# Kernel tuning notes

Measured on AMD Instinct MI355X. Metric: run time of the kernel, lower is better.

Reference implementation:

```python
import jax, jax.numpy as jnp
import numpy as np

N_NODES = 50000
N_EDGES = 800000
IN_DIM = 64
HID = 64
NUM_GRAPHS = 512


def _gcn_conv(x, W, b, row, col, norm, n):
    # PyG GCNConv: h = x @ W; out[col] += norm * h[row]; out += b
    h = x @ W  # [N, HID]
    msg = h[row] * norm[:, None]  # [E', HID]
    out = jax.ops.segment_sum(msg, col, num_segments=n)
    return out + b


def setup_inputs() -> dict:
    key = jax.random.key(0)
    ks = jax.random.split(key, 12)
    x = jax.random.normal(ks[0], (N_NODES, IN_DIM), dtype=jnp.float32)
    edge_index = jax.random.randint(ks[1], (2, N_EDGES), 0, N_NODES, dtype=jnp.int64)
    batch = jnp.sort(jax.random.randint(ks[2], (N_NODES,), 0, NUM_GRAPHS, dtype=jnp.int64))
    s = 0.05
    W1 = jax.random.normal(ks[3], (IN_DIM, HID), dtype=jnp.float32) * s
    b1 = jnp.zeros((HID,), dtype=jnp.float32)
    W2 = jax.random.normal(ks[4], (HID, HID), dtype=jnp.float32) * s
    b2 = jnp.zeros((HID,), dtype=jnp.float32)
    W3 = jax.random.normal(ks[5], (HID, HID), dtype=jnp.float32) * s
    b3 = jnp.zeros((HID,), dtype=jnp.float32)
    lin_W = jax.random.normal(ks[6], (HID, 1), dtype=jnp.float32) * s
    lin_b = jnp.zeros((1,), dtype=jnp.float32)
    return {"x": x, "W1": W1, "b1": b1, "W2": W2, "b2": b2, "W3": W3,
            "b3": b3, "lin_W": lin_W, "lin_b": lin_b,
            "edge_index": edge_index, "batch": batch}


def reference(x, W1, b1, W2, b2, W3, b3, lin_W, lin_b, edge_index, batch):
    n = x.shape[0]
    # add self-loops (GCNConv default add_self_loops=True)
    loop = jnp.arange(n, dtype=edge_index.dtype)
    row = jnp.concatenate([edge_index[0], loop])  # source
    col = jnp.concatenate([edge_index[1], loop])  # target (aggregation index)
    # symmetric degree normalization: deg over targets with unit weights
    deg = jax.ops.segment_sum(jnp.ones_like(col, dtype=x.dtype), col, num_segments=n)
    dinv = jnp.where(deg > 0, jax.lax.rsqrt(deg), 0.0)
    norm = dinv[row] * dinv[col]  # [E+N]

    h = jax.nn.relu(_gcn_conv(x, W1, b1, row, col, norm, n))
    h = jax.nn.relu(_gcn_conv(h, W2, b2, row, col, norm, n))
    h = _gcn_conv(h, W3, b3, row, col, norm, n)

    # global_mean_pool over batch ids
    sums = jax.ops.segment_sum(h, batch, num_segments=NUM_GRAPHS)
    cnt = jax.ops.segment_sum(jnp.ones((n,), dtype=h.dtype), batch, num_segments=NUM_GRAPHS)
    pooled = sums / jnp.maximum(cnt, 1.0)[:, None]
    # dropout p=0.5 is identity in eval mode
    return pooled @ lin_W + lin_b  # [NUM_GRAPHS, 1]
```

## Files before the change

kernel.cpp:

```cpp
#include <hip/hip_runtime.h>
#include <hip/hip_fp16.h>

#define NN 50000
#define NE 800000
#define HD 64
#define NG 512
#define NBK 196
#define NBL 196
#define M_CNT (NBK * NBL)
#define NBS 151
#define GEMM_BLOCKS 3125


__global__ void zero_kernel(int* __restrict__ p, int n) {
    int i = blockIdx.x * blockDim.x + threadIdx.x;
    if (i < n) p[i] = 0;
}

__global__ __launch_bounds__(256) void bucket_count(const int* __restrict__ col,
                                                    const int* __restrict__ batch,
                                                    int* __restrict__ counts,
                                                    int* __restrict__ beg,
                                                    int* __restrict__ endx) {
    __shared__ int hist[256];
    int tid = threadIdx.x, blk = blockIdx.x;
    hist[tid] = 0;
    __syncthreads();
    int base = blk * 4096;
#pragma unroll
    for (int k = 0; k < 16; ++k) {
        int e = base + k * 256 + tid;
        if (e < NE) atomicAdd(&hist[col[e] >> 8], 1);
    }
    int t = blk * 256 + tid;
    if (t < NN) {
        int g = batch[t];
        if (t == 0 || batch[t - 1] != g) beg[g] = t;
        if (t == NN - 1 || batch[t + 1] != g) endx[g] = t + 1;
    }
    __syncthreads();
    if (tid < NBK) counts[tid * NBL + blk] = hist[tid];
}

__global__ __launch_bounds__(256) void block_reduce(const int* __restrict__ src,
                                                    int* __restrict__ bsum) {
    __shared__ int ws[4];
    int tid = threadIdx.x, lane = tid & 63, wid = tid >> 6;
    int i = blockIdx.x * 256 + tid;
    int v = (i < M_CNT) ? src[i] : 0;
#pragma unroll
    for (int off = 32; off > 0; off >>= 1) v += __shfl_down(v, off, 64);
    if (lane == 0) ws[wid] = v;
    __syncthreads();
    if (tid == 0) bsum[blockIdx.x] = ws[0] + ws[1] + ws[2] + ws[3];
}

__global__ __launch_bounds__(64) void scan_bsum(int* __restrict__ bsum) {
    int lane = threadIdx.x;
    int carry = 0;
    for (int base = 0; base < NBS; base += 64) {
        int i = base + lane;
        int v = (i < NBS) ? bsum[i] : 0;
        int inc = v;
#pragma unroll
        for (int off = 1; off < 64; off <<= 1) {
            int t = __shfl_up(inc, off, 64);
            if (lane >= off) inc += t;
        }
        if (i < NBS) bsum[i] = carry + inc - v;
        carry += __shfl(inc, 63, 64);
    }
}

__global__ __launch_bounds__(256) void block_scan(const int* __restrict__ src,
                                                  const int* __restrict__ bsum,
                                                  int* __restrict__ dst) {
    __shared__ int ws[4];
    int tid = threadIdx.x, lane = tid & 63, wid = tid >> 6;
    int i = blockIdx.x * 256 + tid;
    int v = (i < M_CNT) ? src[i] : 0;
    int inc = v;
#pragma unroll
    for (int off = 1; off < 64; off <<= 1) {
        int t = __shfl_up(inc, off, 64);
        if (lane >= off) inc += t;
    }
    if (lane == 63) ws[wid] = inc;
    __syncthreads();
    int woff = 0;
    for (int k = 0; k < wid; ++k) woff += ws[k];
    if (i < M_CNT) dst[i] = bsum[blockIdx.x] + woff + inc - v;
}

__global__ __launch_bounds__(256) void gemm1_scatter(const float* __restrict__ x,
                                                     const float* __restrict__ W1,
                                                     __half* __restrict__ h16,
                                                     const int* __restrict__ row,
                                                     const int* __restrict__ col,
                                                     const int* __restrict__ counts_ex,
                                                     unsigned* __restrict__ packed) {
    if (blockIdx.x < GEMM_BLOCKS) {
        __shared__ float Ws[64][64];
        __shared__ float Is[16][64];
        int t = threadIdx.x;
        for (int i = t; i < 64 * 64; i += 256) Ws[i >> 6][i & 63] = W1[i];
        int row0 = blockIdx.x * 16;
        for (int i = t; i < 16 * 64; i += 256)
            Is[i >> 6][i & 63] = x[(row0 + (i >> 6)) * HD + (i & 63)];
        __syncthreads();
        int c = t & 63, r4 = t >> 6;
        float a0 = 0.f, a1 = 0.f, a2 = 0.f, a3 = 0.f;
#pragma unroll
        for (int k = 0; k < 64; ++k) {
            float w = Ws[k][c];
            a0 += Is[r4 + 0][k] * w;
            a1 += Is[r4 + 4][k] * w;
            a2 += Is[r4 + 8][k] * w;
            a3 += Is[r4 + 12][k] * w;
        }
        h16[(row0 + r4 + 0) * HD + c] = __float2half(a0);
        h16[(row0 + r4 + 4) * HD + c] = __float2half(a1);
        h16[(row0 + r4 + 8) * HD + c] = __float2half(a2);
        h16[(row0 + r4 + 12) * HD + c] = __float2half(a3);
    } else {
        __shared__ int cur[256];
        int tid = threadIdx.x, blk = blockIdx.x - GEMM_BLOCKS;
        cur[tid] = 0;
        __syncthreads();
        int base = blk * 4096;
#pragma unroll
        for (int k = 0; k < 16; ++k) {
            int e = base + k * 256 + tid;
            if (e < NE) {
                int c = col[e], r = row[e];
                int b = c >> 8;
                int lpos = atomicAdd(&cur[b], 1);
                int pos = counts_ex[b * NBL + blk] + lpos;
                packed[pos] = (unsigned)r | ((unsigned)(c & 255) << 16);
            }
        }
    }
}

__global__ __launch_bounds__(256) void csr_rowptr(const unsigned* __restrict__ packed,
                                                  const int* __restrict__ counts_ex,
                                                  int* __restrict__ rowptr,
                                                  float* __restrict__ dinv) {
    __shared__ int hist[256];
    __shared__ int ws[4];
    int bkt = blockIdx.x, tid = threadIdx.x;
    int s = counts_ex[bkt * NBL];
    int e = (bkt == NBK - 1) ? NE : counts_ex[(bkt + 1) * NBL];
    hist[tid] = 0;
    __syncthreads();
    for (int j = s + tid; j < e; j += 256)
        atomicAdd(&hist[(packed[j] >> 16) & 255], 1);
    __syncthreads();
    int lane = tid & 63, wid = tid >> 6;
    int v = hist[tid], inc = v;
#pragma unroll
    for (int off = 1; off < 64; off <<= 1) {
        int t = __shfl_up(inc, off, 64);
        if (lane >= off) inc += t;
    }
    if (lane == 63) ws[wid] = inc;
    __syncthreads();
    int woff = 0;
    for (int k = 0; k < wid; ++k) woff += ws[k];
    int node = bkt * 256 + tid;
    if (node < NN) {
        rowptr[node] = s + woff + inc - v;
        dinv[node] = rsqrtf((float)(v + 1));
    }
    if (bkt == 0 && tid == 0) rowptr[NN] = NE;
}

__global__ __launch_bounds__(256) void csr_fill(const unsigned* __restrict__ packed,
                                                const int* __restrict__ counts_ex,
                                                const int* __restrict__ rowptr,
                                                int* __restrict__ esrc) {
    __shared__ int cur[256];
    int bkt = blockIdx.x, tid = threadIdx.x;
    int s = counts_ex[bkt * NBL];
    int e = (bkt == NBK - 1) ? NE : counts_ex[(bkt + 1) * NBL];
    cur[tid] = 0;
    __syncthreads();
    for (int j = s + tid; j < e; j += 256) {
        unsigned p = packed[j];
        int lc = (p >> 16) & 255;
        int slot = rowptr[(bkt << 8) | lc] + atomicAdd(&cur[lc], 1);
        esrc[slot] = (int)(p & 0xFFFF);
    }
}

__global__ __launch_bounds__(256) void gemm64_f16(const __half* __restrict__ in,
                                                  const float* __restrict__ W,
                                                  __half* __restrict__ out) {
    __shared__ float Ws[64][64];
    __shared__ float Is[16][64];
    int t = threadIdx.x;
    for (int i = t; i < 64 * 64; i += 256) Ws[i >> 6][i & 63] = W[i];
    int row0 = blockIdx.x * 16;
    const __half2* in2 = (const __half2*)(in + (size_t)row0 * HD);
    for (int i = t; i < 16 * 32; i += 256) {
        float2 v = __half22float2(in2[i]);
        int r = i >> 5, c2 = (i & 31) * 2;
        Is[r][c2]     = fmaxf(v.x, 0.f);
        Is[r][c2 + 1] = fmaxf(v.y, 0.f);
    }
    __syncthreads();
    int c = t & 63, r4 = t >> 6;
    float a0 = 0.f, a1 = 0.f, a2 = 0.f, a3 = 0.f;
#pragma unroll
    for (int k = 0; k < 64; ++k) {
        float w = Ws[k][c];
        a0 += Is[r4 + 0][k] * w;
        a1 += Is[r4 + 4][k] * w;
        a2 += Is[r4 + 8][k] * w;
        a3 += Is[r4 + 12][k] * w;
    }
    out[(row0 + r4 + 0) * HD + c] = __float2half(a0);
    out[(row0 + r4 + 4) * HD + c] = __float2half(a1);
    out[(row0 + r4 + 8) * HD + c] = __float2half(a2);
    out[(row0 + r4 + 12) * HD + c] = __float2half(a3);
}

template <bool POOL>
__global__ __launch_bounds__(256) void gather_s(const __half* __restrict__ hp,
                                                const int* __restrict__ rowptr,
                                                const int* __restrict__ esrc,
                                                const float* __restrict__ dinv,
                                                const float* __restrict__ b,
                                                __half* __restrict__ out16,
                                                const int* __restrict__ batch,
                                                float* __restrict__ pooled) {
    int tid = threadIdx.x, lane = tid & 63, wid = tid >> 6;
    int hh = lane >> 5, c = lane & 31;
    int node = blockIdx.x * 4 + wid;
    const __half2* hv = (const __half2*)hp;
    int s = rowptr[node], e = rowptr[node + 1];
    int deg = e - s;
    float2 acc = {0.f, 0.f};
    for (int k = 0; k < deg; k += 64) {
        int my = esrc[s + k + lane] & 0xFFFF;
        float myw = dinv[my];
        int nk = min(deg - k, 64);
        int nmain = nk >> 3;
        for (int j = 0; j < nmain; ++j) {
            int t = j * 8 + hh;
            int s0 = __shfl(my, t, 64);
            int s1 = __shfl(my, t + 2, 64);
            int s2 = __shfl(my, t + 4, 64);
            int s3 = __shfl(my, t + 6, 64);
            float w0 = __shfl(myw, t, 64);
            float w1 = __shfl(myw, t + 2, 64);
            float w2 = __shfl(myw, t + 4, 64);
            float w3 = __shfl(myw, t + 6, 64);
            float2 f0 = __half22float2(hv[s0 * 32 + c]);
            float2 f1 = __half22float2(hv[s1 * 32 + c]);
            float2 f2 = __half22float2(hv[s2 * 32 + c]);
            float2 f3 = __half22float2(hv[s3 * 32 + c]);
            acc.x += w0 * f0.x + w1 * f1.x + w2 * f2.x + w3 * f3.x;
            acc.y += w0 * f0.y + w1 * f1.y + w2 * f2.y + w3 * f3.y;
        }
        int tbase = (nk & ~7) + hh;
#pragma unroll
        for (int u = 0; u < 4; ++u) {
            int t = tbase + 2 * u;
            int sl = __shfl(my, t & 63, 64);
            float w = __shfl(myw, t & 63, 64);
            float wm = (t < nk) ? w : 0.f;
            float2 f = __half22float2(hv[sl * 32 + c]);
            acc.x += wm * f.x;
            acc.y += wm * f.y;
        }
    }
    acc.x += __shfl_xor(acc.x, 32, 64);
    acc.y += __shfl_xor(acc.y, 32, 64);
    if (hh == 0) {
        float di = dinv[node];
        float2 self = __half22float2(hv[node * 32 + c]);
        float2 bb = ((const float2*)b)[c];
        float vx = di * acc.x + di * di * self.x + bb.x;
        float vy = di * acc.y + di * di * self.y + bb.y;
        if (POOL) {
            int g = batch[node];
            atomicAdd(&pooled[g * HD + 2 * c], vx);
            atomicAdd(&pooled[g * HD + 2 * c + 1], vy);
        } else {
            ((__half2*)out16)[node * 32 + c] = __floats2half2_rn(vx, vy);
        }
    }
}

__global__ __launch_bounds__(64) void final_kernel(const float* __restrict__ pooled,
                                                   const int* __restrict__ beg,
                                                   const int* __restrict__ endx,
                                                   const float* __restrict__ lin_W,
                                                   const float* __restrict__ lin_b,
                                                   float* __restrict__ out) {
    int g = blockIdx.x, d = threadIdx.x;
    float cnt = (float)(endx[g] - beg[g]);
    float v = pooled[g * HD + d] / fmaxf(cnt, 1.f) * lin_W[d];
#pragma unroll
    for (int off = 32; off > 0; off >>= 1) v += __shfl_down(v, off, 64);
    if (d == 0) out[g] = v + lin_b[0];
}

extern "C" void kernel_launch(void* const* d_in, const int* in_sizes, int n_in,
                              void* d_out, int out_size, void* d_ws, size_t ws_size,
                              hipStream_t stream) {
    const float* x     = (const float*)d_in[0];
    const float* W1    = (const float*)d_in[1];
    const float* b1    = (const float*)d_in[2];
    const float* W2    = (const float*)d_in[3];
    const float* b2    = (const float*)d_in[4];
    const float* W3    = (const float*)d_in[5];
    const float* b3    = (const float*)d_in[6];
    const float* lin_W = (const float*)d_in[7];
    const float* lin_b = (const float*)d_in[8];
    const int* edge_index = (const int*)d_in[9];
    const int* batch      = (const int*)d_in[10];
    const int* row = edge_index;
    const int* col = edge_index + NE;
    float* out = (float*)d_out;

    __half*   h16       = (__half*)d_ws;
    __half*   A16       = h16 + (size_t)NN * HD;
    int*      esrc      = (int*)(A16 + (size_t)NN * HD);
    unsigned* packed    = (unsigned*)(esrc + NE + 64);
    int*      counts    = (int*)(packed + NE);
    int*      counts_ex = counts + M_CNT;
    int*      rowptr    = counts_ex + M_CNT;
    float*    dinv      = (float*)(rowptr + NN + 2);
    int*      bsum      = (int*)(dinv + NN);
    float*    pooled    = (float*)(bsum + 256);
    int*      beg       = (int*)(pooled + NG * HD);
    int*      endx      = beg + NG;

    const int ZN = NG * HD + 2 * NG;
    zero_kernel<<<(ZN + 255) / 256, 256, 0, stream>>>((int*)pooled, ZN);
    zero_kernel<<<1, 64, 0, stream>>>(esrc + NE, 64);

    bucket_count<<<NBL, 256, 0, stream>>>(col, batch, counts, beg, endx);
    block_reduce<<<NBS, 256, 0, stream>>>(counts, bsum);
    scan_bsum<<<1, 64, 0, stream>>>(bsum);
    block_scan<<<NBS, 256, 0, stream>>>(counts, bsum, counts_ex);
    gemm1_scatter<<<GEMM_BLOCKS + NBL, 256, 0, stream>>>(x, W1, h16, row, col,
                                                         counts_ex, packed);
    csr_rowptr<<<NBK, 256, 0, stream>>>(packed, counts_ex, rowptr, dinv);
    csr_fill<<<NBK, 256, 0, stream>>>(packed, counts_ex, rowptr, esrc);

    const int GB = NN / 4;

    gather_s<false><<<GB, 256, 0, stream>>>(h16, rowptr, esrc, dinv, b1, A16,
                                            batch, pooled);
    gemm64_f16<<<GEMM_BLOCKS, 256, 0, stream>>>(A16, W2, h16);
    gather_s<false><<<GB, 256, 0, stream>>>(h16, rowptr, esrc, dinv, b2, A16,
                                            batch, pooled);
    gemm64_f16<<<GEMM_BLOCKS, 256, 0, stream>>>(A16, W3, h16);
    gather_s<true><<<GB, 256, 0, stream>>>(h16, rowptr, esrc, dinv, b3, nullptr,
                                           batch, pooled);

    final_kernel<<<NG, 64, 0, stream>>>(pooled, beg, endx, lin_W, lin_b, out);
}
```

Baseline: 271.3 us.

## Fuse CSR rowptr/fill kernels, merge zeroing, use scalar-loaded edge lists in gather

Merges csr_rowptr and csr_fill into a single csr_build kernel that keeps the local row pointers in shared memory, so the bucket is read once per phase without an extra launch or a global rowptr reload. The two zeroing launches become one. The gather kernel drops the per-64-edge lane load and shuffle broadcast: the node index is made wave-uniform with readfirstlane, so esrc and dinv become uniform loads and each half-wave selects alternating neighbours. This risks more dependent scalar load latency per 8-edge step in place of the shuffles.

```diff
diff --git a/kernel.cpp b/kernel.cpp
--- a/kernel.cpp
+++ b/kernel.cpp
@@ -12,9 +12,10 @@
 #define GEMM_BLOCKS 3125
 
 
-__global__ void zero_kernel(int* __restrict__ p, int n) {
+__global__ void zero_kernel(int* __restrict__ p, int n, int* __restrict__ q) {
     int i = blockIdx.x * blockDim.x + threadIdx.x;
     if (i < n) p[i] = 0;
+    if (i < 64) q[i] = 0;
 }
 
 __global__ __launch_bounds__(256) void bucket_count(const int* __restrict__ col,
@@ -142,12 +143,14 @@
     }
 }
 
-__global__ __launch_bounds__(256) void csr_rowptr(const unsigned* __restrict__ packed,
-                                                  const int* __restrict__ counts_ex,
-                                                  int* __restrict__ rowptr,
-                                                  float* __restrict__ dinv) {
+__global__ __launch_bounds__(256) void csr_build(const unsigned* __restrict__ packed,
+                                                 const int* __restrict__ counts_ex,
+                                                 int* __restrict__ rowptr,
+                                                 float* __restrict__ dinv,
+                                                 int* __restrict__ esrc) {
     __shared__ int hist[256];
     __shared__ int ws[4];
+    __shared__ int lrp[256];
     int bkt = blockIdx.x, tid = threadIdx.x;
     int s = counts_ex[bkt * NBL];
     int e = (bkt == NBK - 1) ? NE : counts_ex[(bkt + 1) * NBL];
@@ -167,28 +170,20 @@
     __syncthreads();
     int woff = 0;
     for (int k = 0; k < wid; ++k) woff += ws[k];
+    int excl = s + woff + inc - v;
     int node = bkt * 256 + tid;
     if (node < NN) {
-        rowptr[node] = s + woff + inc - v;
+        rowptr[node] = excl;
         dinv[node] = rsqrtf((float)(v + 1));
     }
     if (bkt == 0 && tid == 0) rowptr[NN] = NE;
-}
-
-__global__ __launch_bounds__(256) void csr_fill(const unsigned* __restrict__ packed,
-                                                const int* __restrict__ counts_ex,
-                                                const int* __restrict__ rowptr,
-                                                int* __restrict__ esrc) {
-    __shared__ int cur[256];
-    int bkt = blockIdx.x, tid = threadIdx.x;
-    int s = counts_ex[bkt * NBL];
-    int e = (bkt == NBK - 1) ? NE : counts_ex[(bkt + 1) * NBL];
-    cur[tid] = 0;
+    lrp[tid] = excl;
+    hist[tid] = 0;
     __syncthreads();
     for (int j = s + tid; j < e; j += 256) {
         unsigned p = packed[j];
         int lc = (p >> 16) & 255;
-        int slot = rowptr[(bkt << 8) | lc] + atomicAdd(&cur[lc], 1);
+        int slot = lrp[lc] + atomicAdd(&hist[lc], 1);
         esrc[slot] = (int)(p & 0xFFFF);
     }
 }
@@ -226,58 +221,51 @@
 }
 
 template <bool POOL>
-__global__ __launch_bounds__(256) void gather_s(const __half* __restrict__ hp,
-                                                const int* __restrict__ rowptr,
-                                                const int* __restrict__ esrc,
-                                                const float* __restrict__ dinv,
-                                                const float* __restrict__ b,
-                                                __half* __restrict__ out16,
-                                                const int* __restrict__ batch,
-                                                float* __restrict__ pooled) {
+__global__ __launch_bounds__(256) void gather_sc(const __half* __restrict__ hp,
+                                                 const int* __restrict__ rowptr,
+                                                 const int* __restrict__ esrc,
+                                                 const float* __restrict__ dinv,
+                                                 const float* __restrict__ b,
+                                                 __half* __restrict__ out16,
+                                                 const int* __restrict__ batch,
+                                                 float* __restrict__ pooled) {
     int tid = threadIdx.x, lane = tid & 63, wid = tid >> 6;
-    int hh = lane >> 5, c = lane & 31;
-    int node = blockIdx.x * 4 + wid;
+    int p = lane >> 5, c = lane & 31;
+    int node = __builtin_amdgcn_readfirstlane(blockIdx.x * 4 + wid);
     const __half2* hv = (const __half2*)hp;
     int s = rowptr[node], e = rowptr[node + 1];
-    int deg = e - s;
     float2 acc = {0.f, 0.f};
-    for (int k = 0; k < deg; k += 64) {
-        int my = esrc[s + k + lane] & 0xFFFF;
-        float myw = dinv[my];
-        int nk = min(deg - k, 64);
-        int nmain = nk >> 3;
-        for (int j = 0; j < nmain; ++j) {
-            int t = j * 8 + hh;
-            int s0 = __shfl(my, t, 64);
-            int s1 = __shfl(my, t + 2, 64);
-            int s2 = __shfl(my, t + 4, 64);
-            int s3 = __shfl(my, t + 6, 64);
-            float w0 = __shfl(myw, t, 64);
-            float w1 = __shfl(myw, t + 2, 64);
-            float w2 = __shfl(myw, t + 4, 64);
-            float w3 = __shfl(myw, t + 6, 64);
-            float2 f0 = __half22float2(hv[s0 * 32 + c]);
-            float2 f1 = __half22float2(hv[s1 * 32 + c]);
-            float2 f2 = __half22float2(hv[s2 * 32 + c]);
-            float2 f3 = __half22float2(hv[s3 * 32 + c]);
-            acc.x += w0 * f0.x + w1 * f1.x + w2 * f2.x + w3 * f3.x;
-            acc.y += w0 * f0.y + w1 * f1.y + w2 * f2.y + w3 * f3.y;
-        }
-        int tbase = (nk & ~7) + hh;
-#pragma unroll
-        for (int u = 0; u < 4; ++u) {
-            int t = tbase + 2 * u;
-            int sl = __shfl(my, t & 63, 64);
-            float w = __shfl(myw, t & 63, 64);
-            float wm = (t < nk) ? w : 0.f;
-            float2 f = __half22float2(hv[sl * 32 + c]);
-            acc.x += wm * f.x;
-            acc.y += wm * f.y;
-        }
+    int j = s;
+    for (; j + 8 <= e; j += 8) {
+        int s0 = esrc[j + 0], s1 = esrc[j + 1], s2 = esrc[j + 2], s3 = esrc[j + 3];
+        int s4 = esrc[j + 4], s5 = esrc[j + 5], s6 = esrc[j + 6], s7 = esrc[j + 7];
+        float w0 = dinv[s0], w1 = dinv[s1], w2 = dinv[s2], w3 = dinv[s3];
+        float w4 = dinv[s4], w5 = dinv[s5], w6 = dinv[s6], w7 = dinv[s7];
+        int a0 = p ? s1 : s0;  float u0 = p ? w1 : w0;
+        int a1 = p ? s3 : s2;  float u1 = p ? w3 : w2;
+        int a2 = p ? s5 : s4;  float u2 = p ? w5 : w4;
+        int a3 = p ? s7 : s6;  float u3 = p ? w7 : w6;
+        float2 f0 = __half22float2(hv[a0 * 32 + c]);
+        float2 f1 = __half22float2(hv[a1 * 32 + c]);
+        float2 f2 = __half22float2(hv[a2 * 32 + c]);
+        float2 f3 = __half22float2(hv[a3 * 32 + c]);
+        acc.x += u0 * f0.x + u1 * f1.x + u2 * f2.x + u3 * f3.x;
+        acc.y += u0 * f0.y + u1 * f1.y + u2 * f2.y + u3 * f3.y;
+    }
+    for (; j < e; j += 2) {
+        int s0 = esrc[j];
+        int s1 = (j + 1 < e) ? esrc[j + 1] : s0;
+        float w0 = dinv[s0];
+        float w1 = (j + 1 < e) ? dinv[s1] : 0.f;
+        int a = p ? s1 : s0;
+        float u = p ? w1 : w0;
+        float2 f = __half22float2(hv[a * 32 + c]);
+        acc.x += u * f.x;
+        acc.y += u * f.y;
     }
     acc.x += __shfl_xor(acc.x, 32, 64);
     acc.y += __shfl_xor(acc.y, 32, 64);
-    if (hh == 0) {
+    if (p == 0) {
         float di = dinv[node];
         float2 self = __half22float2(hv[node * 32 + c]);
         float2 bb = ((const float2*)b)[c];
@@ -339,8 +327,7 @@
     int*      endx      = beg + NG;
 
     const int ZN = NG * HD + 2 * NG;
-    zero_kernel<<<(ZN + 255) / 256, 256, 0, stream>>>((int*)pooled, ZN);
-    zero_kernel<<<1, 64, 0, stream>>>(esrc + NE, 64);
+    zero_kernel<<<(ZN + 255) / 256, 256, 0, stream>>>((int*)pooled, ZN, esrc + NE);
 
     bucket_count<<<NBL, 256, 0, stream>>>(col, batch, counts, beg, endx);
     block_reduce<<<NBS, 256, 0, stream>>>(counts, bsum);
@@ -348,19 +335,18 @@
     block_scan<<<NBS, 256, 0, stream>>>(counts, bsum, counts_ex);
     gemm1_scatter<<<GEMM_BLOCKS + NBL, 256, 0, stream>>>(x, W1, h16, row, col,
                                                          counts_ex, packed);
-    csr_rowptr<<<NBK, 256, 0, stream>>>(packed, counts_ex, rowptr, dinv);
-    csr_fill<<<NBK, 256, 0, stream>>>(packed, counts_ex, rowptr, esrc);
+    csr_build<<<NBK, 256, 0, stream>>>(packed, counts_ex, rowptr, dinv, esrc);
 
     const int GB = NN / 4;
 
-    gather_s<false><<<GB, 256, 0, stream>>>(h16, rowptr, esrc, dinv, b1, A16,
+    gather_sc<false><<<GB, 256, 0, stream>>>(h16, rowptr, esrc, dinv, b1, A16,
+                                             batch, pooled);
+    gemm64_f16<<<GEMM_BLOCKS, 256, 0, stream>>>(A16, W2, h16);
+    gather_sc<false><<<GB, 256, 0, stream>>>(h16, rowptr, esrc, dinv, b2, A16,
+                                             batch, pooled);
+    gemm64_f16<<<GEMM_BLOCKS, 256, 0, stream>>>(A16, W3, h16);
+    gather_sc<true><<<GB, 256, 0, stream>>>(h16, rowptr, esrc, dinv, b3, nullptr,
                                             batch, pooled);
-    gemm64_f16<<<GEMM_BLOCKS, 256, 0, stream>>>(A16, W2, h16);
-    gather_s<false><<<GB, 256, 0, stream>>>(h16, rowptr, esrc, dinv, b2, A16,
-                                            batch, pooled);
-    gemm64_f16<<<GEMM_BLOCKS, 256, 0, stream>>>(A16, W3, h16);
-    gather_s<true><<<GB, 256, 0, stream>>>(h16, rowptr, esrc, dinv, b3, nullptr,
-                                           batch, pooled);
 
     final_kernel<<<NG, 64, 0, stream>>>(pooled, beg, endx, lin_W, lin_b, out);
 }
```

After: 269.3 us. About the same (-0.7%).
